# Optimization experiments

Hardware: AMD Instinct MI355X
Metric: run time of the kernel (lower is better)

## Reference

```python
import jax, jax.numpy as jnp
import numpy as np

B, N, DIM, OUT_C, K_ORDERS = 4096, 17, 512, 3, 3  # K=2 -> 3 Chebyshev orders
EPS = 1e-6


def setup_inputs() -> dict:
    key = jax.random.key(0)
    ks = jax.random.split(key, 7)
    x = jax.random.normal(ks[0], (B, N, DIM), dtype=jnp.float32)
    a = jax.random.uniform(ks[1], (N, N), dtype=jnp.float32)
    adj = 0.5 * (a + a.T)  # symmetric, positive row sums
    c = jax.random.normal(ks[2], (B, 1, DIM), dtype=jnp.float32)
    # adaLN modulation: Linear(dim -> 2*dim)
    W_mod = jax.random.normal(ks[3], (DIM, 2 * DIM), dtype=jnp.float32) * (1.0 / np.sqrt(DIM))
    b_mod = jnp.zeros((2 * DIM,), dtype=jnp.float32)
    # ChebConv weights: [K+1, in_c, out_c] (squeezed broadcast dim), bias [out_c]
    Wg = jax.random.normal(ks[4], (K_ORDERS, DIM, OUT_C), dtype=jnp.float32) * (1.0 / np.sqrt(DIM))
    bg = jnp.zeros((OUT_C,), dtype=jnp.float32)
    return {"x": x, "adj": adj, "c": c, "W_mod": W_mod, "b_mod": b_mod, "Wg": Wg, "bg": bg}


def reference(x, adj, c, W_mod, b_mod, Wg, bg):
    # adaLN modulation: SiLU -> Linear -> chunk into shift/scale along dim=2
    h = jax.nn.silu(c) @ W_mod + b_mod                      # [B, 1, 2*DIM]
    shift, scale = jnp.split(h, 2, axis=2)                  # each [B, 1, DIM]
    # LayerNorm (no affine, eps=1e-6) + modulate
    mu = jnp.mean(x, axis=-1, keepdims=True)
    var = jnp.var(x, axis=-1, keepdims=True)
    xn = (x - mu) * jax.lax.rsqrt(var + EPS)
    xm = xn * (1.0 + scale) + shift                         # [B, N, DIM]
    # Normalized Laplacian: L = I - D^{-1/2} A D^{-1/2}
    d = jax.lax.rsqrt(jnp.sum(adj, axis=-1))                # [N]
    L = jnp.eye(adj.shape[0], dtype=adj.dtype) - d[:, None] * adj * d[None, :]
    # Chebyshev polynomials applied to features: T0=x, T1=Lx, T2=(2L^2 - I)x
    T0 = xm
    T1 = jnp.einsum('nm,bmc->bnc', L, xm)
    T2 = 2.0 * jnp.einsum('nm,bmc->bnc', L, T1) - T0
    # Per-order projections, summed over orders, plus bias
    out = (jnp.einsum('bnc,co->bno', T0, Wg[0])
           + jnp.einsum('bnc,co->bno', T1, Wg[1])
           + jnp.einsum('bnc,co->bno', T2, Wg[2])) + bg     # [B, N, 3]
    return out
```

## Files before the change

kernel.cpp:

```cpp
#include <hip/hip_runtime.h>
#include <hip/hip_bf16.h>
#include <stdint.h>

typedef __attribute__((ext_vector_type(8))) short short8;
typedef __attribute__((ext_vector_type(4))) float f32x4;

#define NBATCH 4096
#define NNODE  17
#define NDIM   512
#define ROWLEN 8704

__device__ __forceinline__ unsigned short f2bf(float f) {
    union { float f; unsigned int u; } v; v.f = f;
    unsigned int r = v.u + 0x7fffu + ((v.u >> 16) & 1u);
    return (unsigned short)(r >> 16);
}
__device__ __forceinline__ unsigned int pk2(unsigned short a, unsigned short b) {
    return (unsigned int)a | ((unsigned int)b << 16);
}
__device__ __forceinline__ float silu_f(float x) {
    return x / (1.0f + __expf(-x));
}

__global__ __launch_bounds__(256) void prep_kernel(
        const float* __restrict__ cin, const float* __restrict__ Wmod,
        const float* __restrict__ adj,
        unsigned short* __restrict__ cb, unsigned short* __restrict__ wbT,
        float* __restrict__ Lw) {
    int bid = blockIdx.x;
    int tid = threadIdx.x;
    if (bid == 0) {
        __shared__ float dsh[17];
        if (tid < 17) {
            float rs = 0.0f;
            #pragma unroll
            for (int j = 0; j < 17; ++j) rs += adj[tid * 17 + j];
            dsh[tid] = rsqrtf(rs);
        }
        __syncthreads();
        for (int e = tid; e < 289; e += 256) {
            int i = e / 17, j = e - i * 17;
            Lw[e] = (i == j ? 1.0f : 0.0f) - dsh[i] * adj[e] * dsh[j];
        }
    } else if (bid < 129) {
        __shared__ float tile[64][65];
        int bt = bid - 1;
        int txt = bt & 15, tyt = bt >> 4;
        int cx = tid & 63, ry = tid >> 6;
        #pragma unroll
        for (int rr = 0; rr < 16; ++rr) {
            int r = ry + rr * 4;
            tile[r][cx] = Wmod[(tyt*64 + r) * 1024 + txt*64 + cx];
        }
        __syncthreads();
        #pragma unroll
        for (int rr = 0; rr < 16; ++rr) {
            int r = ry + rr * 4;
            wbT[(txt*64 + r) * 512 + tyt*64 + cx] = f2bf(tile[cx][r]);
        }
    } else {
        int t = (bid - 129) * 256 + tid;
        const float4* s = reinterpret_cast<const float4*>(cin) + (size_t)t * 2;
        float4 a = s[0], b = s[1];
        uint4 o;
        o.x = pk2(f2bf(silu_f(a.x)), f2bf(silu_f(a.y)));
        o.y = pk2(f2bf(silu_f(a.z)), f2bf(silu_f(a.w)));
        o.z = pk2(f2bf(silu_f(b.x)), f2bf(silu_f(b.y)));
        o.w = pk2(f2bf(silu_f(b.z)), f2bf(silu_f(b.w)));
        *reinterpret_cast<uint4*>(cb + (size_t)t * 8) = o;
    }
}

__global__ __launch_bounds__(256) void gemm_kernel(
        const unsigned short* __restrict__ cb, const unsigned short* __restrict__ wbT,
        const float* __restrict__ b_mod, float* __restrict__ H) {
    int w = threadIdx.x >> 6, l = threadIdx.x & 63;
    int lr = l & 15, lk = (l >> 4) * 8;
    int rowbase = blockIdx.y * 128 + w * 32;
    int colbase = blockIdx.x * 64;
    f32x4 acc[2][4] = {};
    for (int kk = 0; kk < 16; ++kk) {
        int k = kk * 32 + lk;
        short8 a0 = *reinterpret_cast<const short8*>(cb + (size_t)(rowbase + lr) * 512 + k);
        short8 a1 = *reinterpret_cast<const short8*>(cb + (size_t)(rowbase + 16 + lr) * 512 + k);
        #pragma unroll
        for (int j = 0; j < 4; ++j) {
            short8 bv = *reinterpret_cast<const short8*>(wbT + (size_t)(colbase + j*16 + lr) * 512 + k);
            acc[0][j] = __builtin_amdgcn_mfma_f32_16x16x32_bf16(a0, bv, acc[0][j], 0, 0, 0);
            acc[1][j] = __builtin_amdgcn_mfma_f32_16x16x32_bf16(a1, bv, acc[1][j], 0, 0, 0);
        }
    }
    #pragma unroll
    for (int j = 0; j < 4; ++j) {
        int col = colbase + j * 16 + lr;
        float bm = b_mod[col];
        #pragma unroll
        for (int i = 0; i < 2; ++i) {
            int row0 = rowbase + i * 16 + (l >> 4) * 4;
            #pragma unroll
            for (int r = 0; r < 4; ++r)
                H[(size_t)(row0 + r) * 1024 + col] = acc[i][j][r] + bm;
        }
    }
}

__global__ __launch_bounds__(512, 4) void main_kernel(
        const float* __restrict__ x, const float* __restrict__ Lw,
        const float* __restrict__ Wg, const float* __restrict__ bg,
        const float* __restrict__ H, float* __restrict__ out) {
    __shared__ float Wt[9][520];
    __shared__ float L_s[17][20];
    __shared__ float P_s[2][18][12];

    int tid = threadIdx.x;
    int w = tid >> 6, l = tid & 63;
    int b0 = blockIdx.x * 2;

    float xv[5][8];
    int tslot[5], tnode[5];
    #pragma unroll
    for (int i = 0; i < 5; ++i) {
        int t = w + i * 8;
        int tc = t < 36 ? t : 35;
        int slot = tc >= 18 ? 1 : 0;
        int node = tc - slot * 18;
        tslot[i] = slot; tnode[i] = node;
        const float* src = (node < 17)
            ? x + (size_t)(b0 + slot) * ROWLEN + node * 512 + 8 * l
            : H + (size_t)(b0 + slot) * 1024 + 8 * l;
        float4 a = reinterpret_cast<const float4*>(src)[0];
        float4 c4 = reinterpret_cast<const float4*>(src)[1];
        xv[i][0]=a.x;  xv[i][1]=a.y;  xv[i][2]=a.z;  xv[i][3]=a.w;
        xv[i][4]=c4.x; xv[i][5]=c4.y; xv[i][6]=c4.z; xv[i][7]=c4.w;
    }
    float fs0[8], fs1[8];
    {
        const float4* h0 = reinterpret_cast<const float4*>(H + (size_t)b0 * 1024 + 512 + 8 * l);
        const float4* h1 = reinterpret_cast<const float4*>(H + (size_t)(b0 + 1) * 1024 + 512 + 8 * l);
        float4 a = h0[0], b = h0[1], c4 = h1[0], d4 = h1[1];
        fs0[0]=1.f+a.x; fs0[1]=1.f+a.y; fs0[2]=1.f+a.z; fs0[3]=1.f+a.w;
        fs0[4]=1.f+b.x; fs0[5]=1.f+b.y; fs0[6]=1.f+b.z; fs0[7]=1.f+b.w;
        fs1[0]=1.f+c4.x; fs1[1]=1.f+c4.y; fs1[2]=1.f+c4.z; fs1[3]=1.f+c4.w;
        fs1[4]=1.f+d4.x; fs1[5]=1.f+d4.y; fs1[6]=1.f+d4.z; fs1[7]=1.f+d4.w;
    }

    {
        int c = tid;
        #pragma unroll
        for (int k = 0; k < 3; ++k) {
            float w0 = Wg[k * 1536 + c * 3 + 0];
            float w1 = Wg[k * 1536 + c * 3 + 1];
            float w2 = Wg[k * 1536 + c * 3 + 2];
            Wt[k * 3 + 0][c] = w0;
            Wt[k * 3 + 1][c] = w1;
            Wt[k * 3 + 2][c] = w2;
        }
    }
    if (tid < 289) {
        int i2 = tid / 17, j2 = tid - i2 * 17;
        L_s[i2][j2] = Lw[tid];
    }
    __syncthreads();

    #pragma unroll
    for (int i = 0; i < 5; ++i) {
        int t = w + i * 8;
        if (t < 36) {
            float xs[8];
            if (tnode[i] < 17) {
                float s = 0.0f, s2 = 0.0f;
                #pragma unroll
                for (int j = 0; j < 8; ++j) { s += xv[i][j]; s2 += xv[i][j] * xv[i][j]; }
                #pragma unroll
                for (int m = 1; m < 64; m <<= 1) { s += __shfl_xor(s, m); s2 += __shfl_xor(s2, m); }
                float mu = s * (1.0f / 512.0f);
                float var = s2 * (1.0f / 512.0f) - mu * mu;
                float rstd = rsqrtf(var + 1e-6f);
                #pragma unroll
                for (int j = 0; j < 8; ++j) {
                    float fj = tslot[i] ? fs1[j] : fs0[j];
                    xs[j] = (xv[i][j] - mu) * rstd * fj;
                }
            } else {
                #pragma unroll
                for (int j = 0; j < 8; ++j) xs[j] = xv[i][j];
            }
            float p[9];
            #pragma unroll
            for (int r = 0; r < 9; ++r) {
                float4 w0 = *reinterpret_cast<const float4*>(&Wt[r][8 * l]);
                float4 w1 = *reinterpret_cast<const float4*>(&Wt[r][8 * l + 4]);
                p[r] = xs[0]*w0.x + xs[1]*w0.y + xs[2]*w0.z + xs[3]*w0.w
                     + xs[4]*w1.x + xs[5]*w1.y + xs[6]*w1.z + xs[7]*w1.w;
            }
            #pragma unroll
            for (int m = 1; m < 64; m <<= 1) {
                #pragma unroll
                for (int r = 0; r < 9; ++r) p[r] += __shfl_xor(p[r], m);
            }
            if (l == 0) {
                #pragma unroll
                for (int r = 0; r < 9; ++r) P_s[tslot[i]][tnode[i]][r] = p[r];
            }
        }
    }
    __syncthreads();

    if (tid < 102) {
        int slot = tid / 51, q = tid - slot * 51;
        int n = q / 3, o = q - n * 3;
        float s2v = P_s[slot][17][6 + o];
        float acc = 0.0f;
        #pragma unroll
        for (int m = 0; m < 17; ++m) acc += L_s[n][m] * (P_s[slot][m][6 + o] + s2v);
        P_s[slot][n][9 + o] = acc;
    }
    __syncthreads();

    if (tid < 102) {
        int slot = tid / 51, q = tid - slot * 51;
        int n = q / 3, o = q - n * 3;
        float s0v = P_s[slot][17][o];
        float s1v = P_s[slot][17][3 + o];
        float s2v = P_s[slot][17][6 + o];
        float r = P_s[slot][n][o] + s0v - P_s[slot][n][6 + o] - s2v + bg[o];
        #pragma unroll
        for (int m = 0; m < 17; ++m)
            r += L_s[n][m] * (P_s[slot][m][3 + o] + s1v + 2.0f * P_s[slot][m][9 + o]);
        out[(size_t)(b0 + slot) * 51 + q] = r;
    }
}

extern "C" void kernel_launch(void* const* d_in, const int* in_sizes, int n_in,
                              void* d_out, int out_size, void* d_ws, size_t ws_size,
                              hipStream_t stream) {
    const float* x     = (const float*)d_in[0];
    const float* adj   = (const float*)d_in[1];
    const float* c     = (const float*)d_in[2];
    const float* W_mod = (const float*)d_in[3];
    const float* b_mod = (const float*)d_in[4];
    const float* Wg    = (const float*)d_in[5];
    const float* bg    = (const float*)d_in[6];
    float* out = (float*)d_out;

    unsigned short* cb  = (unsigned short*)d_ws;
    unsigned short* wbT = (unsigned short*)((char*)d_ws + (4u << 20));
    float*          H   = (float*)((char*)d_ws + (5u << 20));
    float*          Lw  = (float*)((char*)d_ws + (21u << 20));

    prep_kernel<<<1153, 256, 0, stream>>>(c, W_mod, adj, cb, wbT, Lw);
    gemm_kernel<<<dim3(16, 32), 256, 0, stream>>>(cb, wbT, b_mod, H);
    main_kernel<<<2048, 512, 0, stream>>>(x, Lw, Wg, bg, H, out);
}
```

Before: 294.5 us.

## Split main kernel into MFMA projection pass and per-batch combine kernel

The LayerNorm-modulate-project step is rewritten algebraically. Each row's raw x*scale is projected with a bf16 MFMA onto the 9 Chebyshev weight columns, and the row's mean and rstd are stored in a workspace. A separate combine kernel then folds in the mean, rstd, shift and scale projections and applies the Laplacian twice per batch. This removes the heavy per-row shuffle reductions of the old fused kernel and streams x in a coalesced row layout. In exchange it adds an extra launch and a workspace round trip, and the bf16 inputs to the dot product reduce precision.

```diff
diff --git a/kernel.cpp b/kernel.cpp
--- a/kernel.cpp
+++ b/kernel.cpp
@@ -5,9 +5,6 @@
 typedef __attribute__((ext_vector_type(8))) short short8;
 typedef __attribute__((ext_vector_type(4))) float f32x4;
 
-#define NBATCH 4096
-#define NNODE  17
-#define NDIM   512
 #define ROWLEN 8704
 
 __device__ __forceinline__ unsigned short f2bf(float f) {
@@ -20,6 +17,10 @@
 }
 __device__ __forceinline__ float silu_f(float x) {
     return x / (1.0f + __expf(-x));
+}
+__device__ __forceinline__ float sel3(float a, float b, float c, int o) {
+    float r = (o == 1) ? b : a;
+    return (o == 2) ? c : r;
 }
 
 __global__ __launch_bounds__(256) void prep_kernel(
@@ -104,131 +105,164 @@
     }
 }
 
-__global__ __launch_bounds__(512, 4) void main_kernel(
-        const float* __restrict__ x, const float* __restrict__ Lw,
-        const float* __restrict__ Wg, const float* __restrict__ bg,
-        const float* __restrict__ H, float* __restrict__ out) {
-    __shared__ float Wt[9][520];
+__global__ __launch_bounds__(512, 3) void mainA_kernel(
+        const float* __restrict__ x, const float* __restrict__ Wg,
+        const float* __restrict__ H, float* __restrict__ Gw) {
+    __shared__ float scl[9][520];
+
+    int tid = threadIdx.x, w = tid >> 6, l = tid & 63;
+    int R0 = blockIdx.x * 128;
+    int b_lo = R0 / 17;
+
+    #pragma unroll
+    for (int bi = 0; bi < 9; ++bi) {
+        int b = b_lo + bi; if (b > 4095) b = 4095;
+        scl[bi][tid] = 1.0f + H[(size_t)b * 1024 + 512 + tid];
+    }
+
+    int col = l & 15, q = l >> 4;
+    bool bvalid = col < 9;
+    int cheb = col / 3, oo = col - cheb * 3;
+    const float* wgbase = Wg + cheb * 1536 + oo;
+    short8 bf[16];
+    #pragma unroll
+    for (int kk = 0; kk < 16; ++kk) {
+        unsigned short t[8];
+        #pragma unroll
+        for (int j = 0; j < 8; ++j) {
+            int c = kk * 32 + q * 8 + j;
+            float v = bvalid ? wgbase[c * 3] : 0.0f;
+            t[j] = f2bf(v);
+        }
+        uint4 uv;
+        uv.x = pk2(t[0], t[1]); uv.y = pk2(t[2], t[3]);
+        uv.z = pk2(t[4], t[5]); uv.w = pk2(t[6], t[7]);
+        bf[kk] = *reinterpret_cast<short8*>(&uv);
+    }
+    __syncthreads();
+
+    int myrow = R0 + w * 16 + col;
+    int bi = myrow / 17 - b_lo;
+    const float* xrow = x + (size_t)myrow * 512 + q * 8;
+    const float* srow = &scl[bi][q * 8];
+
+    float sum = 0.0f, sumsq = 0.0f;
+    f32x4 acc = {0.f, 0.f, 0.f, 0.f};
+    #pragma unroll
+    for (int kk = 0; kk < 16; ++kk) {
+        float4 xa = *reinterpret_cast<const float4*>(xrow + kk * 32);
+        float4 xb = *reinterpret_cast<const float4*>(xrow + kk * 32 + 4);
+        float4 sa = *reinterpret_cast<const float4*>(srow + kk * 32);
+        float4 sb = *reinterpret_cast<const float4*>(srow + kk * 32 + 4);
+        sum  += xa.x + xa.y + xa.z + xa.w + xb.x + xb.y + xb.z + xb.w;
+        sumsq = fmaf(xa.x, xa.x, sumsq); sumsq = fmaf(xa.y, xa.y, sumsq);
+        sumsq = fmaf(xa.z, xa.z, sumsq); sumsq = fmaf(xa.w, xa.w, sumsq);
+        sumsq = fmaf(xb.x, xb.x, sumsq); sumsq = fmaf(xb.y, xb.y, sumsq);
+        sumsq = fmaf(xb.z, xb.z, sumsq); sumsq = fmaf(xb.w, xb.w, sumsq);
+        uint4 uv;
+        uv.x = pk2(f2bf(xa.x * sa.x), f2bf(xa.y * sa.y));
+        uv.y = pk2(f2bf(xa.z * sa.z), f2bf(xa.w * sa.w));
+        uv.z = pk2(f2bf(xb.x * sb.x), f2bf(xb.y * sb.y));
+        uv.w = pk2(f2bf(xb.z * sb.z), f2bf(xb.w * sb.w));
+        short8 av = *reinterpret_cast<short8*>(&uv);
+        acc = __builtin_amdgcn_mfma_f32_16x16x32_bf16(av, bf[kk], acc, 0, 0, 0);
+    }
+
+    sum   += __shfl_xor(sum, 16);   sum   += __shfl_xor(sum, 32);
+    sumsq += __shfl_xor(sumsq, 16); sumsq += __shfl_xor(sumsq, 32);
+    float mu  = sum * (1.0f / 512.0f);
+    float var = sumsq * (1.0f / 512.0f) - mu * mu;
+    float rstd = rsqrtf(var + 1e-6f);
+
+    size_t gbase = (size_t)(R0 + w * 16);
+    if (bvalid) {
+        #pragma unroll
+        for (int r = 0; r < 4; ++r)
+            Gw[(gbase + q * 4 + r) * 12 + col] = acc[r];
+    }
+    if (l < 16) {
+        Gw[(gbase + l) * 12 + 9]  = mu;
+        Gw[(gbase + l) * 12 + 10] = rstd;
+    }
+}
+
+__global__ __launch_bounds__(512) void combine_kernel(
+        const float* __restrict__ H, const float* __restrict__ Wg,
+        const float* __restrict__ Lw, const float* __restrict__ bg,
+        const float* __restrict__ Gw, float* __restrict__ out) {
+    __shared__ float Wt_t[9][512];
     __shared__ float L_s[17][20];
-    __shared__ float P_s[2][18][12];
-
-    int tid = threadIdx.x;
-    int w = tid >> 6, l = tid & 63;
-    int b0 = blockIdx.x * 2;
-
-    float xv[5][8];
-    int tslot[5], tnode[5];
-    #pragma unroll
-    for (int i = 0; i < 5; ++i) {
-        int t = w + i * 8;
-        int tc = t < 36 ? t : 35;
-        int slot = tc >= 18 ? 1 : 0;
-        int node = tc - slot * 18;
-        tslot[i] = slot; tnode[i] = node;
-        const float* src = (node < 17)
-            ? x + (size_t)(b0 + slot) * ROWLEN + node * 512 + 8 * l
-            : H + (size_t)(b0 + slot) * 1024 + 8 * l;
-        float4 a = reinterpret_cast<const float4*>(src)[0];
-        float4 c4 = reinterpret_cast<const float4*>(src)[1];
-        xv[i][0]=a.x;  xv[i][1]=a.y;  xv[i][2]=a.z;  xv[i][3]=a.w;
-        xv[i][4]=c4.x; xv[i][5]=c4.y; xv[i][6]=c4.z; xv[i][7]=c4.w;
-    }
-    float fs0[8], fs1[8];
-    {
-        const float4* h0 = reinterpret_cast<const float4*>(H + (size_t)b0 * 1024 + 512 + 8 * l);
-        const float4* h1 = reinterpret_cast<const float4*>(H + (size_t)(b0 + 1) * 1024 + 512 + 8 * l);
-        float4 a = h0[0], b = h0[1], c4 = h1[0], d4 = h1[1];
-        fs0[0]=1.f+a.x; fs0[1]=1.f+a.y; fs0[2]=1.f+a.z; fs0[3]=1.f+a.w;
-        fs0[4]=1.f+b.x; fs0[5]=1.f+b.y; fs0[6]=1.f+b.z; fs0[7]=1.f+b.w;
-        fs1[0]=1.f+c4.x; fs1[1]=1.f+c4.y; fs1[2]=1.f+c4.z; fs1[3]=1.f+c4.w;
-        fs1[4]=1.f+d4.x; fs1[5]=1.f+d4.y; fs1[6]=1.f+d4.z; fs1[7]=1.f+d4.w;
-    }
-
-    {
+    __shared__ float A2_s[8][17][3];
+    __shared__ float B1_s[8][17][3];
+
+    int tid = threadIdx.x, w = tid >> 6, l = tid & 63;
+
+    #pragma unroll
+    for (int r = 0; r < 9; ++r) {
         int c = tid;
-        #pragma unroll
-        for (int k = 0; k < 3; ++k) {
-            float w0 = Wg[k * 1536 + c * 3 + 0];
-            float w1 = Wg[k * 1536 + c * 3 + 1];
-            float w2 = Wg[k * 1536 + c * 3 + 2];
-            Wt[k * 3 + 0][c] = w0;
-            Wt[k * 3 + 1][c] = w1;
-            Wt[k * 3 + 2][c] = w2;
-        }
-    }
-    if (tid < 289) {
-        int i2 = tid / 17, j2 = tid - i2 * 17;
-        L_s[i2][j2] = Lw[tid];
-    }
-    __syncthreads();
-
-    #pragma unroll
-    for (int i = 0; i < 5; ++i) {
-        int t = w + i * 8;
-        if (t < 36) {
-            float xs[8];
-            if (tnode[i] < 17) {
-                float s = 0.0f, s2 = 0.0f;
-                #pragma unroll
-                for (int j = 0; j < 8; ++j) { s += xv[i][j]; s2 += xv[i][j] * xv[i][j]; }
-                #pragma unroll
-                for (int m = 1; m < 64; m <<= 1) { s += __shfl_xor(s, m); s2 += __shfl_xor(s2, m); }
-                float mu = s * (1.0f / 512.0f);
-                float var = s2 * (1.0f / 512.0f) - mu * mu;
-                float rstd = rsqrtf(var + 1e-6f);
-                #pragma unroll
-                for (int j = 0; j < 8; ++j) {
-                    float fj = tslot[i] ? fs1[j] : fs0[j];
-                    xs[j] = (xv[i][j] - mu) * rstd * fj;
-                }
-            } else {
-                #pragma unroll
-                for (int j = 0; j < 8; ++j) xs[j] = xv[i][j];
-            }
-            float p[9];
-            #pragma unroll
-            for (int r = 0; r < 9; ++r) {
-                float4 w0 = *reinterpret_cast<const float4*>(&Wt[r][8 * l]);
-                float4 w1 = *reinterpret_cast<const float4*>(&Wt[r][8 * l + 4]);
-                p[r] = xs[0]*w0.x + xs[1]*w0.y + xs[2]*w0.z + xs[3]*w0.w
-                     + xs[4]*w1.x + xs[5]*w1.y + xs[6]*w1.z + xs[7]*w1.w;
-            }
-            #pragma unroll
-            for (int m = 1; m < 64; m <<= 1) {
-                #pragma unroll
-                for (int r = 0; r < 9; ++r) p[r] += __shfl_xor(p[r], m);
-            }
-            if (l == 0) {
-                #pragma unroll
-                for (int r = 0; r < 9; ++r) P_s[tslot[i]][tnode[i]][r] = p[r];
-            }
-        }
-    }
-    __syncthreads();
-
-    if (tid < 102) {
-        int slot = tid / 51, q = tid - slot * 51;
-        int n = q / 3, o = q - n * 3;
-        float s2v = P_s[slot][17][6 + o];
-        float acc = 0.0f;
-        #pragma unroll
-        for (int m = 0; m < 17; ++m) acc += L_s[n][m] * (P_s[slot][m][6 + o] + s2v);
-        P_s[slot][n][9 + o] = acc;
-    }
-    __syncthreads();
-
-    if (tid < 102) {
-        int slot = tid / 51, q = tid - slot * 51;
-        int n = q / 3, o = q - n * 3;
-        float s0v = P_s[slot][17][o];
-        float s1v = P_s[slot][17][3 + o];
-        float s2v = P_s[slot][17][6 + o];
-        float r = P_s[slot][n][o] + s0v - P_s[slot][n][6 + o] - s2v + bg[o];
-        #pragma unroll
-        for (int m = 0; m < 17; ++m)
-            r += L_s[n][m] * (P_s[slot][m][3 + o] + s1v + 2.0f * P_s[slot][m][9 + o]);
-        out[(size_t)(b0 + slot) * 51 + q] = r;
-    }
+        Wt_t[r][(c & 7) * 64 + (c >> 3)] = Wg[(r / 3) * 1536 + c * 3 + (r % 3)];
+    }
+    if (tid < 289) L_s[tid / 17][tid % 17] = Lw[tid];
+    __syncthreads();
+
+    int b = blockIdx.x * 8 + w;
+    const float* hrow = H + (size_t)b * 1024;
+    float4 h0 = *reinterpret_cast<const float4*>(hrow + 8 * l);
+    float4 h1 = *reinterpret_cast<const float4*>(hrow + 8 * l + 4);
+    float4 h2 = *reinterpret_cast<const float4*>(hrow + 512 + 8 * l);
+    float4 h3 = *reinterpret_cast<const float4*>(hrow + 512 + 8 * l + 4);
+    float shj[8] = {h0.x, h0.y, h0.z, h0.w, h1.x, h1.y, h1.z, h1.w};
+    float scj[8] = {1.f+h2.x, 1.f+h2.y, 1.f+h2.z, 1.f+h2.w,
+                    1.f+h3.x, 1.f+h3.y, 1.f+h3.z, 1.f+h3.w};
+
+    float sA[9], cA[9];
+    #pragma unroll
+    for (int r = 0; r < 9; ++r) {
+        float s = 0.0f, cs = 0.0f;
+        #pragma unroll
+        for (int j = 0; j < 8; ++j) {
+            float wv = Wt_t[r][j * 64 + l];
+            s  = fmaf(shj[j], wv, s);
+            cs = fmaf(scj[j], wv, cs);
+        }
+        sA[r] = s; cA[r] = cs;
+    }
+    #pragma unroll
+    for (int m = 1; m < 64; m <<= 1) {
+        #pragma unroll
+        for (int r = 0; r < 9; ++r) {
+            sA[r] += __shfl_xor(sA[r], m);
+            cA[r] += __shfl_xor(cA[r], m);
+        }
+    }
+
+    int lc = l < 51 ? l : 50;
+    int n = lc / 3, o = lc - n * 3;
+    float S0 = sel3(sA[0], sA[1], sA[2], o);
+    float S1 = sel3(sA[3], sA[4], sA[5], o);
+    float S2 = sel3(sA[6], sA[7], sA[8], o);
+    float C0 = sel3(cA[0], cA[1], cA[2], o);
+    float C1 = sel3(cA[3], cA[4], cA[5], o);
+    float C2 = sel3(cA[6], cA[7], cA[8], o);
+
+    const float* grow = Gw + (size_t)(b * 17 + n) * 12;
+    float g0 = grow[o], g1 = grow[3 + o], g2 = grow[6 + o];
+    float mu = grow[9], rstd = grow[10];
+    float A0 = rstd * (g0 - mu * C0) + S0;
+    float A1 = rstd * (g1 - mu * C1) + S1;
+    float A2 = rstd * (g2 - mu * C2) + S2;
+
+    A2_s[w][n][o] = A2;
+    __syncthreads();
+    float Qv = 0.0f;
+    #pragma unroll
+    for (int m = 0; m < 17; ++m) Qv = fmaf(L_s[n][m], A2_s[w][m][o], Qv);
+    B1_s[w][n][o] = A1 + 2.0f * Qv;
+    __syncthreads();
+    float rv = A0 - A2 + bg[o];
+    #pragma unroll
+    for (int m = 0; m < 17; ++m) rv = fmaf(L_s[n][m], B1_s[w][m][o], rv);
+    if (l < 51) out[(size_t)b * 51 + lc] = rv;
 }
 
 extern "C" void kernel_launch(void* const* d_in, const int* in_sizes, int n_in,
@@ -247,8 +281,10 @@
     unsigned short* wbT = (unsigned short*)((char*)d_ws + (4u << 20));
     float*          H   = (float*)((char*)d_ws + (5u << 20));
     float*          Lw  = (float*)((char*)d_ws + (21u << 20));
+    float*          Gw  = (float*)((char*)d_ws + (22u << 20));
 
     prep_kernel<<<1153, 256, 0, stream>>>(c, W_mod, adj, cb, wbT, Lw);
     gemm_kernel<<<dim3(16, 32), 256, 0, stream>>>(cb, wbT, b_mod, H);
-    main_kernel<<<2048, 512, 0, stream>>>(x, Lw, Wg, bg, H, out);
-}
+    mainA_kernel<<<544, 512, 0, stream>>>(x, Wg, H, Gw);
+    combine_kernel<<<512, 512, 0, stream>>>(H, Wg, Lw, bg, Gw, out);
+}
```

Result: no change. 298.7 us (+1.4%).
